# Kernel tuning notes

Measured on AMD Instinct MI355X. Metric: run time of the kernel, lower is better.

The kernel has to match this reference:

```python
import jax, jax.numpy as jnp
import numpy as np

B = 32          # decode batch
H = 32          # query heads (TP shard)
KV_LORA = 512   # latent dim
ROPE = 64       # rope head dim
NOPE = 128      # nope head dim
VH = 128        # v head dim
QL = 1536       # q lora rank
HID = 5120      # model hidden
BLK = 128       # page/block size
BLOCKS_PER_SEQ = 32   # 4096-token context
NB = B * BLOCKS_PER_SEQ
CACHE_BLOCKS = 1200


def _rope(x, pos):
    # x: [B, n, ROPE] (neox half-rotation), pos: [B] int positions
    half = x.shape[-1] // 2
    inv = 1.0 / (10000.0 ** (jnp.arange(half, dtype=jnp.float32) / half))
    ang = pos.astype(jnp.float32)[:, None] * inv              # [B, half]
    cos, sin = jnp.cos(ang)[:, None, :], jnp.sin(ang)[:, None, :]
    x1, x2 = x[..., :half], x[..., half:]
    return jnp.concatenate([x1 * cos - x2 * sin, x2 * cos + x1 * sin], axis=-1)


def setup_inputs() -> dict:
    key = jax.random.key(0)
    ks = jax.random.split(key, 10)
    inp = {
        'hidden_states_or_q_c': jax.random.normal(ks[0], (B, QL), jnp.float32),
        'k_c_normed': jax.random.normal(ks[1], (B, 1, KV_LORA), jnp.float32),
        'k_pe': jax.random.normal(ks[2], (B, 1, ROPE), jnp.float32),
        'kv_cache_k': jax.random.normal(ks[3], (CACHE_BLOCKS, BLK, ROPE), jnp.float32),
        'kv_cache_v': jax.random.normal(ks[4], (CACHE_BLOCKS, BLK, KV_LORA), jnp.float32),
        'W_Q': jax.random.normal(ks[5], (QL, H * NOPE), jnp.float32) / np.sqrt(QL),
        'W_UK': jax.random.normal(ks[6], (H, NOPE, KV_LORA), jnp.float32) / np.sqrt(NOPE),
        'W_QR': jax.random.normal(ks[7], (QL, H * ROPE), jnp.float32) / np.sqrt(QL),
        'W_UV': jax.random.normal(ks[8], (H, KV_LORA, VH), jnp.float32) / np.sqrt(KV_LORA),
        'W_O': jax.random.normal(ks[9], (H * VH, HID), jnp.float32) / np.sqrt(H * VH),
        'input_positions': jnp.full((B,), BLK * BLOCKS_PER_SEQ - 1, jnp.int32),
        'block_list': jnp.arange(NB, dtype=jnp.int32),
        'block_groups': (jnp.arange(NB, dtype=jnp.int32) // BLOCKS_PER_SEQ),
        'block_bias': jnp.zeros((NB, BLK), jnp.float32),
        'block_indices': (jnp.arange(B, dtype=jnp.int32) * BLOCKS_PER_SEQ + BLOCKS_PER_SEQ - 1),
        'block_offsets': jnp.full((B,), BLK - 1, jnp.int32),
    }
    inp['block_mapping'] = jax.nn.one_hot(inp['block_groups'], B, dtype=jnp.float32)
    return inp


def reference(hidden_states_or_q_c, k_c_normed, k_pe, kv_cache_k, kv_cache_v,
              W_Q, W_UK, W_QR, W_UV, W_O,
              input_positions, block_list, block_groups, block_mapping,
              block_bias, block_indices, block_offsets):
    b = hidden_states_or_q_c.shape[0]
    h, nope, kv_lora = W_UK.shape
    rope = k_pe.shape[-1]
    scale = 1.0 / np.sqrt(nope + rope)

    # absorbed q projection: q_nope in latent space (_q_proj_and_k_up_proj)
    q_nope = jnp.einsum('bq,qhd->bhd', hidden_states_or_q_c, W_Q.reshape(-1, h, nope))
    q_nope = jnp.einsum('bhd,hdl->bhl', q_nope, W_UK)          # [B,H,kv_lora]
    q_pe = (hidden_states_or_q_c @ W_QR).reshape(b, h, rope)
    pos = input_positions.reshape(b)
    q_pe = _rope(q_pe, pos)
    k_pe_r = _rope(k_pe, pos)                                  # [B,1,rope]

    # write new latent token into paged cache (latent_cache_k / latent_cache_v)
    kv_cache_k = kv_cache_k.at[block_indices, block_offsets].set(k_pe_r[:, 0, :])
    kv_cache_v = kv_cache_v.at[block_indices, block_offsets].set(k_c_normed[:, 0, :])

    # flat_pa_mla: query [B,H,kv_lora+rope], key = concat(value_latent, k_pe)
    q = jnp.concatenate([q_nope, q_pe], axis=-1) * scale       # [B,H,576]
    keys = kv_cache_k[block_list]                              # [NB,BLK,rope]
    vals = kv_cache_v[block_list]                              # [NB,BLK,kv_lora]
    kcat = jnp.concatenate([vals, keys], axis=-1)              # [NB,BLK,576]

    qb = jnp.einsum('nb,bhd->nhd', block_mapping, q)           # batch2block
    logits = jnp.einsum('nhd,nkd->nhk', qb, kcat) + block_bias[:, None, :]

    # grouped (per-batch) softmax across this batch's blocks == pipelined_pa math
    gmax = jax.ops.segment_max(logits.max(-1), block_groups, num_segments=b)  # [B,H]
    p = jnp.exp(logits - gmax[block_groups][:, :, None])       # [NB,H,BLK]
    av = jnp.einsum('nhk,nkl->nhl', p, vals)                   # [NB,H,kv_lora]
    num = jnp.einsum('nb,nhl->bhl', block_mapping, av)         # block2batch
    den = jnp.einsum('nb,nh->bh', block_mapping, p.sum(-1))
    attn = num / den[..., None]                                # [B,H,kv_lora]

    # _v_up_proj_and_o_proj
    out = jnp.einsum('bhl,hlv->bhv', attn, W_UV).reshape(b, -1) @ W_O
    return out.reshape(b, 1, -1)
```

## Files before the change

### kernel.cpp

```cpp
#include <hip/hip_runtime.h>
#include <stdint.h>


typedef __attribute__((ext_vector_type(8))) short short8;
typedef __attribute__((ext_vector_type(4))) float f32x4;

__device__ inline uint32_t f2bf(float f) {
  uint32_t u = __float_as_uint(f);
  return (u + 0x7fffu + ((u >> 16) & 1u)) >> 16;
}
__device__ inline uint32_t pack2bf(float lo, float hi) {
  return f2bf(lo) | (f2bf(hi) << 16);
}
union FragU { uint32_t u[4]; short8 s; };
__device__ inline short8 frag_from(const uint32_t r[4]) {
  FragU v; v.u[0] = r[0]; v.u[1] = r[1]; v.u[2] = r[2]; v.u[3] = r[3];
  return v.s;
}

__global__ __launch_bounds__(256) void k1_qproj(
    const float* __restrict__ hidden, const float* __restrict__ W_Q,
    const float* __restrict__ W_QR, float* __restrict__ q_nope0,
    float* __restrict__ q_pe0) {
  __shared__ float hl[32][129];
  const int t = threadIdx.x;
  const int ctile = blockIdx.x * 128;
  const int k0 = blockIdx.y * 128;
  const bool isQ = (ctile < 4096);
  const float* W = isQ ? W_Q : W_QR;
  const int wstride = isQ ? 4096 : 2048;
  const int c = (isQ ? ctile : ctile - 4096) + (t & 31) * 4;
  const int rg = t >> 5;
  for (int idx = t; idx < 4096; idx += 256) {
    int b = idx >> 7, kk = idx & 127;
    hl[b][kk] = hidden[b * 1536 + k0 + kk];
  }
  __syncthreads();
  float acc[4][4];
#pragma unroll
  for (int r = 0; r < 4; ++r)
#pragma unroll
    for (int j = 0; j < 4; ++j) acc[r][j] = 0.f;
  const float* wp = W + (size_t)k0 * wstride + c;
#pragma unroll 4
  for (int kk = 0; kk < 128; ++kk) {
    float4 w = *(const float4*)wp;
    wp += wstride;
#pragma unroll
    for (int r = 0; r < 4; ++r) {
      float hv = hl[rg * 4 + r][kk];
      acc[r][0] += hv * w.x;
      acc[r][1] += hv * w.y;
      acc[r][2] += hv * w.z;
      acc[r][3] += hv * w.w;
    }
  }
  float* dst = isQ ? q_nope0 : q_pe0;
#pragma unroll
  for (int r = 0; r < 4; ++r)
#pragma unroll
    for (int j = 0; j < 4; ++j)
      atomicAdd(&dst[(rg * 4 + r) * wstride + c + j], acc[r][j]);
}

__global__ __launch_bounds__(256) void k2_qlora(
    const float* __restrict__ q_nope0, const float* __restrict__ W_UK,
    float* __restrict__ q_acc) {
  __shared__ float qn[32][65];
  const int t = threadIdx.x;
  const int h = blockIdx.y;
  const int c0 = blockIdx.x * 128;
  const int d0 = blockIdx.z * 64;
  for (int idx = t; idx < 2048; idx += 256) {
    int b = idx >> 6, dd = idx & 63;
    qn[b][dd] = q_nope0[b * 4096 + h * 128 + d0 + dd];
  }
  __syncthreads();
  const int c = c0 + (t & 31) * 4;
  const int rg = t >> 5;
  float acc[4][4];
#pragma unroll
  for (int r = 0; r < 4; ++r)
#pragma unroll
    for (int j = 0; j < 4; ++j) acc[r][j] = 0.f;
  const float* wp = W_UK + (size_t)(h * 128 + d0) * 512 + c;
#pragma unroll 4
  for (int dd = 0; dd < 64; ++dd) {
    float4 w = *(const float4*)wp;
    wp += 512;
#pragma unroll
    for (int r = 0; r < 4; ++r) {
      float qv = qn[rg * 4 + r][dd];
      acc[r][0] += qv * w.x;
      acc[r][1] += qv * w.y;
      acc[r][2] += qv * w.z;
      acc[r][3] += qv * w.w;
    }
  }
#pragma unroll
  for (int r = 0; r < 4; ++r)
#pragma unroll
    for (int j = 0; j < 4; ++j)
      atomicAdd(&q_acc[(size_t)((rg * 4 + r) * 32 + h) * 512 + c + j],
                acc[r][j]);
}

__global__ __launch_bounds__(256) void k2b_rope_scatter(
    const float* __restrict__ q_pe0, const float* __restrict__ k_pe,
    const float* __restrict__ k_c_normed, const int* __restrict__ ipos,
    const int* __restrict__ bindices, const int* __restrict__ boffsets,
    const float* __restrict__ q_acc, float* __restrict__ cache_k,
    float* __restrict__ cache_v, uint16_t* __restrict__ q_bf) {
  const int b = blockIdx.x;
  const int t = threadIdx.x;
  const float pos = (float)ipos[b];
  const float scale = 0.07216878364870323f;
  const float lnk = 0.28782313662425575f;
  for (int idx = t; idx < 16384; idx += 256) {
    int h = idx >> 9, c = idx & 511;
    q_bf[((size_t)b * 32 + h) * 576 + c] =
        (uint16_t)f2bf(q_acc[((size_t)b * 32 + h) * 512 + c] * scale);
  }
  for (int idx = t; idx < 1024; idx += 256) {
    int h = idx >> 5, i = idx & 31;
    float ang = pos * __expf(-(float)i * lnk);
    float s, c;
    sincosf(ang, &s, &c);
    float x1 = q_pe0[b * 2048 + h * 64 + i];
    float x2 = q_pe0[b * 2048 + h * 64 + 32 + i];
    int base = (b * 32 + h) * 576 + 512;
    q_bf[base + i]      = (uint16_t)f2bf((x1 * c - x2 * s) * scale);
    q_bf[base + 32 + i] = (uint16_t)f2bf((x2 * c + x1 * s) * scale);
  }
  const int row = bindices[b] * 128 + boffsets[b];
  if (t < 32) {
    int i = t;
    float ang = pos * __expf(-(float)i * lnk);
    float s, c;
    sincosf(ang, &s, &c);
    float x1 = k_pe[b * 64 + i], x2 = k_pe[b * 64 + 32 + i];
    cache_k[row * 64 + i]      = x1 * c - x2 * s;
    cache_k[row * 64 + 32 + i] = x2 * c + x1 * s;
  }
  for (int j = t; j < 512; j += 256)
    cache_v[row * 512 + j] = k_c_normed[b * 512 + j];
}

__global__ __launch_bounds__(256, 2) void k3_attn(
    const uint16_t* __restrict__ q_bf, const float* __restrict__ cache_k,
    const float* __restrict__ cache_v, const int* __restrict__ block_list,
    const int* __restrict__ block_groups, const float* __restrict__ block_bias,
    float* __restrict__ num_part, float* __restrict__ den_part) {
  __shared__ uint32_t Tl[288 * 33];
  __shared__ uint32_t Pl[16 * 33];
  __shared__ float den_sh[2][32];

  const int t = threadIdx.x;
  const int part = blockIdx.x, bseq = blockIdx.y;
  const int wg = bseq * 16 + part;
  const int wave = t >> 6, lane = t & 63, quad = lane >> 4, l16 = lane & 15;
  const int hh = wave >> 1, kvh = wave & 1;
  const int n0 = bseq * 32 + part * 2;
  const int g = block_groups[n0];

  uint32_t qf[72];
  {
    const uint32_t* qrow =
        (const uint32_t*)(q_bf + (size_t)(g * 32 + hh * 16 + l16) * 576);
#pragma unroll
    for (int ks = 0; ks < 18; ++ks)
#pragma unroll
      for (int i = 0; i < 4; ++i)
        qf[ks * 4 + i] = qrow[ks * 16 + quad * 4 + i];
  }

  const f32x4 fzero = {0.f, 0.f, 0.f, 0.f};
  f32x4 acc[2][8];
#pragma unroll
  for (int mt = 0; mt < 2; ++mt)
#pragma unroll
    for (int nt = 0; nt < 8; ++nt) acc[mt][nt] = fzero;
  float den_acc[4] = {0.f, 0.f, 0.f, 0.f};

  for (int blk_i = 0; blk_i < 2; ++blk_i) {
    const int n = n0 + blk_i;
    const int phys = block_list[n];
    const float* vrow = cache_v + (size_t)phys * 128 * 512;
    const float* krow = cache_k + (size_t)phys * 128 * 64;
    for (int s = 0; s < 4; ++s) {
      const int s0 = s * 32;
      __syncthreads();
      for (int idx = t; idx < 4608; idx += 256) {
        int kv = idx / 144, f4 = idx - kv * 144;
        float4 v; int d0;
        if (f4 < 128) { v = *(const float4*)(vrow + (s0 + kv) * 512 + f4 * 4); d0 = f4 * 4; }
        else { v = *(const float4*)(krow + (s0 + kv) * 64 + (f4 - 128) * 4); d0 = 512 + (f4 - 128) * 4; }
        int d2 = d0 >> 1;
        Tl[(d2    ) * 33 + kv] = pack2bf(v.x, v.y);
        Tl[(d2 + 1) * 33 + kv] = pack2bf(v.z, v.w);
      }
      __syncthreads();
      const int tkv = kvh * 16 + l16;
      f32x4 lg = fzero;
#pragma unroll
      for (int ks = 0; ks < 18; ++ks) {
        uint32_t br[4];
#pragma unroll
        for (int i = 0; i < 4; ++i)
          br[i] = Tl[(ks * 16 + quad * 4 + i) * 33 + tkv];
        lg = __builtin_amdgcn_mfma_f32_16x16x32_bf16(
            frag_from(&qf[ks * 4]), frag_from(br), lg, 0, 0, 0);
      }
      float bias = block_bias[n * 128 + s0 + tkv];
      uint32_t pb[4];
#pragma unroll
      for (int r = 0; r < 4; ++r) {
        float p = __expf(lg[r] + bias);
        pb[r] = f2bf(p);
        den_acc[r] += __uint_as_float(pb[r] << 16);
      }
#pragma unroll
      for (int r = 0; r < 4; ++r) {
        uint32_t other = (uint32_t)__shfl_xor((int)pb[r], 1, 64);
        if ((l16 & 1) == 0) {
          int h = hh * 16 + quad * 4 + r;
          Pl[(tkv >> 1) * 33 + h] = pb[r] | (other << 16);
        }
      }
      __syncthreads();
      uint32_t af[2][4];
#pragma unroll
      for (int mt = 0; mt < 2; ++mt)
#pragma unroll
        for (int i = 0; i < 4; ++i)
          af[mt][i] = Pl[(quad * 4 + i) * 33 + mt * 16 + l16];
#pragma unroll
      for (int nt = 0; nt < 8; ++nt) {
        int l = wave * 128 + nt * 16 + l16;
        const uint32_t* base = &Tl[(l >> 1) * 33 + quad * 8];
        uint32_t dw[8];
#pragma unroll
        for (int j = 0; j < 8; ++j) dw[j] = base[j];
        uint32_t br[4];
        const bool odd = (l & 1);
#pragma unroll
        for (int i = 0; i < 4; ++i) {
          uint32_t a = dw[2 * i], bq = dw[2 * i + 1];
          uint32_t lo = odd ? (a >> 16) : (a & 0xffffu);
          uint32_t hi = odd ? (bq & 0xffff0000u) : (bq << 16);
          br[i] = lo | hi;
        }
        short8 bf = frag_from(br);
        acc[0][nt] = __builtin_amdgcn_mfma_f32_16x16x32_bf16(
            frag_from(af[0]), bf, acc[0][nt], 0, 0, 0);
        acc[1][nt] = __builtin_amdgcn_mfma_f32_16x16x32_bf16(
            frag_from(af[1]), bf, acc[1][nt], 0, 0, 0);
      }
    }
  }
#pragma unroll
  for (int mt = 0; mt < 2; ++mt)
#pragma unroll
    for (int nt = 0; nt < 8; ++nt)
#pragma unroll
      for (int r = 0; r < 4; ++r) {
        int h = mt * 16 + quad * 4 + r;
        int l = wave * 128 + nt * 16 + l16;
        num_part[((size_t)wg * 32 + h) * 512 + l] = acc[mt][nt][r];
      }
  float dv[4];
#pragma unroll
  for (int r = 0; r < 4; ++r) {
    float v = den_acc[r];
    v += __shfl_xor(v, 1, 64);
    v += __shfl_xor(v, 2, 64);
    v += __shfl_xor(v, 4, 64);
    v += __shfl_xor(v, 8, 64);
    dv[r] = v;
  }
  if (l16 == 0) {
#pragma unroll
    for (int r = 0; r < 4; ++r)
      den_sh[kvh][hh * 16 + quad * 4 + r] = dv[r];
  }
  __syncthreads();
  if (t < 32) den_part[wg * 32 + t] = den_sh[0][t] + den_sh[1][t];
}

__global__ __launch_bounds__(256) void k4_reduce_wuv(
    const float* __restrict__ num_part, const float* __restrict__ den_part,
    const float* __restrict__ W_UV, float* __restrict__ o_acc) {
  __shared__ float attn[32][33];
  __shared__ float den[32];
  const int t = threadIdx.x;
  const int lc = blockIdx.x, h = blockIdx.y;
  const int c0 = lc * 32;
  if (t < 32) {
    float s = 0.f;
    for (int p = 0; p < 16; ++p) s += den_part[(t * 16 + p) * 32 + h];
    den[t] = s;
  }
  __syncthreads();
  {
    const int l = t & 31, bg = t >> 5;
    for (int bb = 0; bb < 4; ++bb) {
      int b = bg * 4 + bb;
      float s = 0.f;
#pragma unroll
      for (int p = 0; p < 16; ++p)
        s += num_part[((size_t)(b * 16 + p) * 32 + h) * 512 + c0 + l];
      attn[b][l] = s / den[b];
    }
  }
  __syncthreads();
  const int v = t & 127, rg = t >> 7;
  float acc[16];
#pragma unroll
  for (int r = 0; r < 16; ++r) acc[r] = 0.f;
  for (int l = 0; l < 32; ++l) {
    float w = W_UV[(h * 512 + c0 + l) * 128 + v];
#pragma unroll
    for (int r = 0; r < 16; ++r) acc[r] += attn[rg * 16 + r][l] * w;
  }
  for (int r = 0; r < 16; ++r)
    atomicAdd(&o_acc[(size_t)(rg * 16 + r) * 4096 + h * 128 + v], acc[r]);
}

__global__ __launch_bounds__(256) void k5_wo(
    const float* __restrict__ o_acc, const float* __restrict__ W_O,
    float* __restrict__ out) {
  __shared__ uint32_t Bt[32 * 130];
  const int t = threadIdx.x;
  const int ksplit = blockIdx.x, ntile = blockIdx.y;
  const int n0 = ntile * 128, kbase = ksplit * 256;
  const int wave = t >> 6, lane = t & 63, quad = lane >> 4, l16 = lane & 15;
  const f32x4 fzero = {0.f, 0.f, 0.f, 0.f};
  f32x4 acc[2][2];
#pragma unroll
  for (int mt = 0; mt < 2; ++mt)
#pragma unroll
    for (int nt = 0; nt < 2; ++nt) acc[mt][nt] = fzero;
  for (int kc = 0; kc < 4; ++kc) {
    const int k0 = kbase + kc * 64;
    __syncthreads();
    for (int idx = t; idx < 1024; idx += 256) {
      int k2 = idx >> 5, c4 = idx & 31;
      const float* p0 = &W_O[(size_t)(k0 + 2 * k2) * 5120 + n0 + c4 * 4];
      float4 a = *(const float4*)p0;
      float4 b = *(const float4*)(p0 + 5120);
      uint32_t* bp = &Bt[k2 * 130 + c4 * 4];
      bp[0] = pack2bf(a.x, b.x);
      bp[1] = pack2bf(a.y, b.y);
      bp[2] = pack2bf(a.z, b.z);
      bp[3] = pack2bf(a.w, b.w);
    }
    __syncthreads();
#pragma unroll
    for (int ks2 = 0; ks2 < 2; ++ks2) {
      uint32_t af[2][4];
#pragma unroll
      for (int mt = 0; mt < 2; ++mt) {
        const float* orow =
            o_acc + (size_t)(mt * 16 + l16) * 4096 + k0 + ks2 * 32 + quad * 8;
        float4 x = *(const float4*)orow;
        float4 y = *(const float4*)(orow + 4);
        af[mt][0] = pack2bf(x.x, x.y);
        af[mt][1] = pack2bf(x.z, x.w);
        af[mt][2] = pack2bf(y.x, y.y);
        af[mt][3] = pack2bf(y.z, y.w);
      }
#pragma unroll
      for (int nt = 0; nt < 2; ++nt) {
        uint32_t br[4];
#pragma unroll
        for (int i = 0; i < 4; ++i)
          br[i] = Bt[(ks2 * 16 + quad * 4 + i) * 130 + wave * 32 + nt * 16 + l16];
        short8 bf = frag_from(br);
        acc[0][nt] = __builtin_amdgcn_mfma_f32_16x16x32_bf16(
            frag_from(af[0]), bf, acc[0][nt], 0, 0, 0);
        acc[1][nt] = __builtin_amdgcn_mfma_f32_16x16x32_bf16(
            frag_from(af[1]), bf, acc[1][nt], 0, 0, 0);
      }
    }
  }
#pragma unroll
  for (int mt = 0; mt < 2; ++mt)
#pragma unroll
    for (int nt = 0; nt < 2; ++nt)
#pragma unroll
      for (int r = 0; r < 4; ++r) {
        int b = mt * 16 + quad * 4 + r;
        int c = n0 + wave * 32 + nt * 16 + l16;
        atomicAdd(&out[(size_t)b * 5120 + c], acc[mt][nt][r]);
      }
}

extern "C" void kernel_launch(void* const* d_in, const int* in_sizes, int n_in,
                              void* d_out, int out_size, void* d_ws,
                              size_t ws_size, hipStream_t stream) {
  (void)in_sizes; (void)n_in; (void)ws_size;
  const float* hidden = (const float*)d_in[0];
  const float* k_c    = (const float*)d_in[1];
  const float* k_pe   = (const float*)d_in[2];
  float* cache_k      = (float*)d_in[3];
  float* cache_v      = (float*)d_in[4];
  const float* W_Q    = (const float*)d_in[5];
  const float* W_UK   = (const float*)d_in[6];
  const float* W_QR   = (const float*)d_in[7];
  const float* W_UV   = (const float*)d_in[8];
  const float* W_O    = (const float*)d_in[9];
  const int* ipos     = (const int*)d_in[10];
  const int* blist    = (const int*)d_in[11];
  const int* bgroups  = (const int*)d_in[12];
  const float* bbias  = (const float*)d_in[13];
  const int* bindices = (const int*)d_in[14];
  const int* boffsets = (const int*)d_in[15];

  char* ws = (char*)d_ws;
  float*    q_nope0  = (float*)(ws);
  float*    q_pe0    = (float*)(ws + 524288);
  float*    o_acc    = (float*)(ws + 786432);
  uint16_t* q_bf     = (uint16_t*)(ws + 1310720);
  float*    den_part = (float*)(ws + 2490368);
  float*    num_part = (float*)(ws + 2555904);
  float*    q_acc    = num_part;
  float*    out      = (float*)d_out;

  hipMemsetAsync(ws, 0, 1310720, stream);
  hipMemsetAsync((void*)q_acc, 0, 2097152, stream);
  hipMemsetAsync(d_out, 0, (size_t)out_size * sizeof(float), stream);

  k1_qproj<<<dim3(48, 12), 256, 0, stream>>>(hidden, W_Q, W_QR, q_nope0, q_pe0);
  k2_qlora<<<dim3(4, 32, 2), 256, 0, stream>>>(q_nope0, W_UK, q_acc);
  k2b_rope_scatter<<<32, 256, 0, stream>>>(q_pe0, k_pe, k_c, ipos, bindices,
                                           boffsets, q_acc, cache_k, cache_v,
                                           q_bf);
  k3_attn<<<dim3(16, 32), 256, 0, stream>>>(q_bf, cache_k, cache_v, blist,
                                            bgroups, bbias, num_part, den_part);
  k4_reduce_wuv<<<dim3(16, 32), 256, 0, stream>>>(num_part, den_part, W_UV, o_acc);
  k5_wo<<<dim3(16, 40), 256, 0, stream>>>(o_acc, W_O, out);
}
```

Baseline: 702.7 us.

## Split q-lora and rope-scatter grids wider, vectorize partial reduction, use bf16 intrinsic

```diff
diff --git a/kernel.cpp b/kernel.cpp
--- a/kernel.cpp
+++ b/kernel.cpp
@@ -1,4 +1,5 @@
 #include <hip/hip_runtime.h>
+#include <hip/hip_bf16.h>
 #include <stdint.h>
 
 
@@ -9,8 +10,10 @@
   uint32_t u = __float_as_uint(f);
   return (u + 0x7fffu + ((u >> 16) & 1u)) >> 16;
 }
+union Bf2U { __hip_bfloat162 h; uint32_t u; };
 __device__ inline uint32_t pack2bf(float lo, float hi) {
-  return f2bf(lo) | (f2bf(hi) << 16);
+  Bf2U v; v.h = __float22bfloat162_rn(float2{lo, hi});
+  return v.u;
 }
 union FragU { uint32_t u[4]; short8 s; };
 __device__ inline short8 frag_from(const uint32_t r[4]) {
@@ -66,13 +69,13 @@
 __global__ __launch_bounds__(256) void k2_qlora(
     const float* __restrict__ q_nope0, const float* __restrict__ W_UK,
     float* __restrict__ q_acc) {
-  __shared__ float qn[32][65];
+  __shared__ float qn[32][33];
   const int t = threadIdx.x;
   const int h = blockIdx.y;
   const int c0 = blockIdx.x * 128;
-  const int d0 = blockIdx.z * 64;
-  for (int idx = t; idx < 2048; idx += 256) {
-    int b = idx >> 6, dd = idx & 63;
+  const int d0 = blockIdx.z * 32;
+  for (int idx = t; idx < 1024; idx += 256) {
+    int b = idx >> 5, dd = idx & 31;
     qn[b][dd] = q_nope0[b * 4096 + h * 128 + d0 + dd];
   }
   __syncthreads();
@@ -85,7 +88,7 @@
     for (int j = 0; j < 4; ++j) acc[r][j] = 0.f;
   const float* wp = W_UK + (size_t)(h * 128 + d0) * 512 + c;
 #pragma unroll 4
-  for (int dd = 0; dd < 64; ++dd) {
+  for (int dd = 0; dd < 32; ++dd) {
     float4 w = *(const float4*)wp;
     wp += 512;
 #pragma unroll
@@ -112,17 +115,18 @@
     const float* __restrict__ q_acc, float* __restrict__ cache_k,
     float* __restrict__ cache_v, uint16_t* __restrict__ q_bf) {
   const int b = blockIdx.x;
+  const int hs = blockIdx.y * 4;
   const int t = threadIdx.x;
   const float pos = (float)ipos[b];
   const float scale = 0.07216878364870323f;
   const float lnk = 0.28782313662425575f;
-  for (int idx = t; idx < 16384; idx += 256) {
-    int h = idx >> 9, c = idx & 511;
+  for (int idx = t; idx < 2048; idx += 256) {
+    int h = hs + (idx >> 9), c = idx & 511;
     q_bf[((size_t)b * 32 + h) * 576 + c] =
         (uint16_t)f2bf(q_acc[((size_t)b * 32 + h) * 512 + c] * scale);
   }
-  for (int idx = t; idx < 1024; idx += 256) {
-    int h = idx >> 5, i = idx & 31;
+  if (t < 128) {
+    int h = hs + (t >> 5), i = t & 31;
     float ang = pos * __expf(-(float)i * lnk);
     float s, c;
     sincosf(ang, &s, &c);
@@ -132,18 +136,20 @@
     q_bf[base + i]      = (uint16_t)f2bf((x1 * c - x2 * s) * scale);
     q_bf[base + 32 + i] = (uint16_t)f2bf((x2 * c + x1 * s) * scale);
   }
-  const int row = bindices[b] * 128 + boffsets[b];
-  if (t < 32) {
-    int i = t;
-    float ang = pos * __expf(-(float)i * lnk);
-    float s, c;
-    sincosf(ang, &s, &c);
-    float x1 = k_pe[b * 64 + i], x2 = k_pe[b * 64 + 32 + i];
-    cache_k[row * 64 + i]      = x1 * c - x2 * s;
-    cache_k[row * 64 + 32 + i] = x2 * c + x1 * s;
-  }
-  for (int j = t; j < 512; j += 256)
-    cache_v[row * 512 + j] = k_c_normed[b * 512 + j];
+  if (blockIdx.y == 0) {
+    const int row = bindices[b] * 128 + boffsets[b];
+    if (t < 32) {
+      int i = t;
+      float ang = pos * __expf(-(float)i * lnk);
+      float s, c;
+      sincosf(ang, &s, &c);
+      float x1 = k_pe[b * 64 + i], x2 = k_pe[b * 64 + 32 + i];
+      cache_k[row * 64 + i]      = x1 * c - x2 * s;
+      cache_k[row * 64 + 32 + i] = x2 * c + x1 * s;
+    }
+    for (int j = t; j < 512; j += 256)
+      cache_v[row * 512 + j] = k_c_normed[b * 512 + j];
+  }
 }
 
 __global__ __launch_bounds__(256, 2) void k3_attn(
@@ -302,15 +308,18 @@
   }
   __syncthreads();
   {
-    const int l = t & 31, bg = t >> 5;
-    for (int bb = 0; bb < 4; ++bb) {
-      int b = bg * 4 + bb;
-      float s = 0.f;
-#pragma unroll
-      for (int p = 0; p < 16; ++p)
-        s += num_part[((size_t)(b * 16 + p) * 32 + h) * 512 + c0 + l];
-      attn[b][l] = s / den[b];
-    }
+    const int b = t >> 3, l4 = (t & 7) * 4;
+    float4 s = {0.f, 0.f, 0.f, 0.f};
+#pragma unroll
+    for (int p = 0; p < 16; ++p) {
+      float4 v = *(const float4*)&num_part[((size_t)(b * 16 + p) * 32 + h) * 512 + c0 + l4];
+      s.x += v.x; s.y += v.y; s.z += v.z; s.w += v.w;
+    }
+    float inv = 1.f / den[b];
+    attn[b][l4 + 0] = s.x * inv;
+    attn[b][l4 + 1] = s.y * inv;
+    attn[b][l4 + 2] = s.z * inv;
+    attn[b][l4 + 3] = s.w * inv;
   }
   __syncthreads();
   const int v = t & 127, rg = t >> 7;
@@ -431,10 +440,10 @@
   hipMemsetAsync(d_out, 0, (size_t)out_size * sizeof(float), stream);
 
   k1_qproj<<<dim3(48, 12), 256, 0, stream>>>(hidden, W_Q, W_QR, q_nope0, q_pe0);
-  k2_qlora<<<dim3(4, 32, 2), 256, 0, stream>>>(q_nope0, W_UK, q_acc);
-  k2b_rope_scatter<<<32, 256, 0, stream>>>(q_pe0, k_pe, k_c, ipos, bindices,
-                                           boffsets, q_acc, cache_k, cache_v,
-                                           q_bf);
+  k2_qlora<<<dim3(4, 32, 4), 256, 0, stream>>>(q_nope0, W_UK, q_acc);
+  k2b_rope_scatter<<<dim3(32, 8), 256, 0, stream>>>(q_pe0, k_pe, k_c, ipos,
+                                                    bindices, boffsets, q_acc,
+                                                    cache_k, cache_v, q_bf);
   k3_attn<<<dim3(16, 32), 256, 0, stream>>>(q_bf, cache_k, cache_v, blist,
                                             bgroups, bbias, num_part, den_part);
   k4_reduce_wuv<<<dim3(16, 32), 256, 0, stream>>>(num_part, den_part, W_UV, o_acc);
```

After: 702.4 us. Within noise of the previous version (-0.0%).
